# Kernel tuning notes

Hardware: AMD Instinct MI355X
Metric: run time of the kernel (lower is better)

Reference implementation:

```python
import jax, jax.numpy as jnp
import numpy as np

N, E, D, L, B = 50000, 800000, 128, 3, 256
BN_EPS = 1e-5


def _bn(h, g, b):
    # BatchNorm1d training-mode math over the node axis (biased variance)
    mu = jnp.mean(h, axis=0)
    var = jnp.mean(jnp.square(h - mu), axis=0)
    return (h - mu) * jax.lax.rsqrt(var + BN_EPS) * g + b


def setup_inputs() -> dict:
    key = jax.random.key(0)
    ks = jax.random.split(key, 6)
    scale = 1.0 / np.sqrt(D).astype(np.float32)
    return {
        "x": jax.random.normal(ks[0], (N, D), dtype=jnp.float32),
        "edge_index": jax.random.randint(ks[1], (2, E), 0, N, dtype=jnp.int32),
        "batch": jnp.sort(jax.random.randint(ks[2], (N,), 0, B, dtype=jnp.int32)),
        "W1": jax.random.normal(ks[3], (L, D, D), dtype=jnp.float32) * scale,
        "b1": jnp.zeros((L, D), jnp.float32),
        "g1": jnp.ones((L, D), jnp.float32),
        "be1": jnp.zeros((L, D), jnp.float32),
        "W2": jax.random.normal(ks[4], (L, D, D), dtype=jnp.float32) * scale,
        "b2": jnp.zeros((L, D), jnp.float32),
        "g2": jnp.ones((L, D), jnp.float32),
        "be2": jnp.zeros((L, D), jnp.float32),
    }


def reference(x, edge_index, batch, W1, b1, g1, be1, W2, b2, g2, be2):
    src, dst = edge_index[0], edge_index[1]
    h = x
    for i in range(L):
        # GINConv (eps=0): h' = nn((1+eps)*h + sum_{j in N(i)} h_j)
        agg = jax.ops.segment_sum(h[src], dst, num_segments=N)  # [N, D]
        h = h + agg
        # nn_layer: Linear -> BN -> ReLU -> Linear
        h = jax.nn.relu(_bn(h @ W1[i] + b1[i], g1[i], be1[i])) @ W2[i] + b2[i]
        # outer BatchNorm + ReLU (dropout is identity in eval)
        h = jax.nn.relu(_bn(h, g2[i], be2[i]))
    # global_add_pool over graphs
    return jax.ops.segment_sum(h, batch, num_segments=B)  # [B, D]
```

## Files before the change

kernel.cpp:

```cpp
#include <hip/hip_runtime.h>

constexpr int kN = 50000;
constexpr int kE = 800000;
constexpr int kD = 128;
constexpr int kB = 256;
constexpr int kL = 3;
constexpr float kEps = 1e-5f;

constexpr int kShift = 7;
constexpr int kNBuk = (kN + 127) >> 7;
constexpr int kEPB = 8192;
constexpr int kNBinBlk = (kE + kEPB - 1) / kEPB;

constexpr int kScanN = kN + 1;
constexpr int kScanGrid = (kScanN + 1023) / 1024;

constexpr int kPxc = kN * kD / 8;
constexpr int kPhist = kPxc + kE;
constexpr int kPbnd = kPhist + kN + 1;
constexpr int kPw1 = kPbnd + kL * kD * kD;
constexpr int kPw2 = kPw1 + kL * kD * kD;

typedef __attribute__((ext_vector_type(8))) short short8;
typedef __attribute__((ext_vector_type(4))) float f32x4;

__device__ __forceinline__ float4 bnrelu4(float4 v, float4 sc, float4 sh) {
  float4 r;
  r.x = fmaxf(fmaf(v.x, sc.x, sh.x), 0.f);
  r.y = fmaxf(fmaf(v.y, sc.y, sh.y), 0.f);
  r.z = fmaxf(fmaf(v.z, sc.z, sh.z), 0.f);
  r.w = fmaxf(fmaf(v.w, sc.w, sh.w), 0.f);
  return r;
}

__device__ __forceinline__ void acc4(float4& a, const float4& v) {
  a.x += v.x; a.y += v.y; a.z += v.z; a.w += v.w;
}
__device__ __forceinline__ void accsq4(float4& a, const float4& v) {
  a.x = fmaf(v.x, v.x, a.x); a.y = fmaf(v.y, v.y, a.y);
  a.z = fmaf(v.z, v.z, a.z); a.w = fmaf(v.w, v.w, a.w);
}

__device__ __forceinline__ unsigned int f2bf(float x) {
  unsigned int u = __float_as_uint(x);
  u = u + 0x7FFFu + ((u >> 16) & 1u);
  return u >> 16;
}
__device__ __forceinline__ float bf2f(unsigned int lo16) {
  return __uint_as_float(lo16 << 16);
}

__device__ __forceinline__ void bnmake(float su, float sq, float ga, float be,
                                       float& sc, float& sh) {
  float mu = su * (1.f / kN);
  float var = fmaf(-mu, mu, sq * (1.f / kN));
  float s = ga * rsqrtf(var + kEps);
  sc = s;
  sh = fmaf(-mu, s, be);
}

__global__ void k_prep(const float* __restrict__ x, const int* __restrict__ ei,
                       const int* __restrict__ bat, const float* __restrict__ W1,
                       const float* __restrict__ W2,
                       unsigned short* __restrict__ x16, int* __restrict__ rowptr,
                       int* __restrict__ gstart, unsigned short* __restrict__ Wf1,
                       unsigned short* __restrict__ Wf2) {
  int idx = blockIdx.x * 256 + threadIdx.x;
  if (idx < kPxc) {
    const float* ap = x + (size_t)idx * 8;
    float4 v0 = *reinterpret_cast<const float4*>(ap);
    float4 v1 = *reinterpret_cast<const float4*>(ap + 4);
    short8 u;
    u[0] = (short)f2bf(v0.x); u[1] = (short)f2bf(v0.y);
    u[2] = (short)f2bf(v0.z); u[3] = (short)f2bf(v0.w);
    u[4] = (short)f2bf(v1.x); u[5] = (short)f2bf(v1.y);
    u[6] = (short)f2bf(v1.z); u[7] = (short)f2bf(v1.w);
    *reinterpret_cast<short8*>(x16 + (size_t)idx * 8) = u;
  } else if (idx < kPhist) {
    int e = idx - kPxc;
    atomicAdd(&rowptr[1 + ei[kE + e]], 1);
  } else if (idx < kPbnd) {
    int n = idx - kPhist;
    int b = (n < kN) ? bat[n] : kB;
    int bp = (n > 0) ? bat[n - 1] : -1;
    for (int g = bp + 1; g <= b; ++g) gstart[g] = n;
  } else if (idx < kPw2) {
    const float* W = (idx < kPw1) ? W1 : W2;
    unsigned short* Wf = (idx < kPw1) ? Wf1 : Wf2;
    int id2 = idx - ((idx < kPw1) ? kPbnd : kPw1);
    int m = id2 & (kD * kD - 1);
    int w = id2 >> 14;
    int k = m >> 7, col = m & 127;
    int kb = k >> 5, cb = col >> 4;
    int lane = (col & 15) + 16 * ((k & 31) >> 3);
    int j = k & 7;
    Wf[(size_t)w * kD * kD + ((size_t)(kb * 8 + cb) * 64 + lane) * 8 + j] =
        (unsigned short)f2bf(W[id2]);
  }
}

__global__ __launch_bounds__(256) void k_scanA(int* __restrict__ data,
                                               int* __restrict__ partial) {
  __shared__ int wsum[4];
  const int tid = threadIdx.x;
  const int lane = tid & 63, wid = tid >> 6;
  const int base = blockIdx.x * 1024 + tid * 4;
  int4 v = make_int4(0, 0, 0, 0);
  if (base + 3 < kScanN) {
    v = *reinterpret_cast<const int4*>(data + base);
  } else if (base < kScanN) {
    v.x = data[base];
    if (base + 1 < kScanN) v.y = data[base + 1];
    if (base + 2 < kScanN) v.z = data[base + 2];
  }
  int s = v.x + v.y + v.z + v.w;
  int inc = s;
#pragma unroll
  for (int off = 1; off < 64; off <<= 1) {
    int t = __shfl_up(inc, off);
    if (lane >= off) inc += t;
  }
  if (lane == 63) wsum[wid] = inc;
  __syncthreads();
  int wpre = 0, total = 0;
#pragma unroll
  for (int k = 0; k < 4; ++k) {
    int t = wsum[k];
    if (k < wid) wpre += t;
    total += t;
  }
  if (tid == 0) partial[blockIdx.x] = total;
  int excl = wpre + inc - s;
  v.x += excl;
  v.y += v.x;
  v.z += v.y;
  v.w += v.z;
  if (base + 3 < kScanN) {
    *reinterpret_cast<int4*>(data + base) = v;
  } else if (base < kScanN) {
    data[base] = v.x;
    if (base + 1 < kScanN) data[base + 1] = v.y;
    if (base + 2 < kScanN) data[base + 2] = v.z;
  }
}

__global__ __launch_bounds__(256) void k_scanC(int* __restrict__ data,
                                               const int* __restrict__ partial,
                                               int* __restrict__ bcur) {
  const int b = blockIdx.x;
  const int tid = threadIdx.x;
  const int lane = tid & 63;
  int p = (lane < b) ? partial[lane] : 0;
#pragma unroll
  for (int off = 32; off; off >>= 1) p += __shfl_down(p, off);
  const int off0 = __shfl(p, 0);
  const int base = b * 1024 + tid * 4;
  if (base + 3 < kScanN) {
    int4 v = *reinterpret_cast<int4*>(data + base);
    v.x += off0; v.y += off0; v.z += off0; v.w += off0;
    *reinterpret_cast<int4*>(data + base) = v;
    if ((tid & 31) == 0) {
      int bk = b * 8 + (tid >> 5);
      if (bk < kNBuk) bcur[bk] = v.x;
    }
  } else if (base < kScanN) {
    for (int j = 0; j < 4 && base + j < kScanN; ++j) data[base + j] += off0;
  }
}

__global__ __launch_bounds__(256) void k_binpairs(
    const int* __restrict__ ei, int* __restrict__ bcur,
    unsigned int* __restrict__ pairs) {
  __shared__ int cnt[kNBuk];
  __shared__ int base[kNBuk];
  const int tid = threadIdx.x;
  const int e0 = blockIdx.x * kEPB;
  for (int t = tid; t < kNBuk; t += 256) cnt[t] = 0;
  __syncthreads();
  unsigned int dr[32];
#pragma unroll
  for (int i = 0; i < 32; ++i) {
    int e = e0 + i * 256 + tid;
    unsigned int v = 0xFFFFFFFFu;
    if (e < kE) {
      int d = ei[kE + e];
      int r = atomicAdd(&cnt[d >> kShift], 1);
      v = ((unsigned int)d << 16) | (unsigned int)r;
    }
    dr[i] = v;
  }
  __syncthreads();
  for (int t = tid; t < kNBuk; t += 256) {
    int c = cnt[t];
    base[t] = (c > 0) ? atomicAdd(&bcur[t], c) : 0;
  }
  __syncthreads();
#pragma unroll
  for (int i = 0; i < 32; ++i) {
    unsigned int v = dr[i];
    if (v == 0xFFFFFFFFu) continue;
    int e = e0 + i * 256 + tid;
    unsigned int s = (unsigned int)ei[e];
    int b = (int)(v >> 16) >> kShift;
    int pos = base[b] + (int)(v & 0xFFFFu);
    pairs[pos] = (v & 0xFFFF0000u) | s;
  }
}

__global__ __launch_bounds__(256) void k_csrfill(
    const unsigned int* __restrict__ pairs, const int* __restrict__ rowptr,
    int* __restrict__ srcs) {
  __shared__ int cur[128];
  const int b = blockIdx.x;
  const int tid = threadIdx.x;
  const int n0 = b << kShift;
  if (tid < 128) {
    int n = n0 + tid;
    cur[tid] = (n < kN) ? rowptr[n] : 0;
  }
  __syncthreads();
  const int pbeg = rowptr[n0];
  const int pend = rowptr[min(n0 + 128, kN)];
  for (int p = pbeg + tid; p < pend; p += 256) {
    unsigned int u = pairs[p];
    int local = (int)(u >> 16) - n0;
    int pos = atomicAdd(&cur[local], 1);
    srcs[pos] = (int)(u & 0xFFFFu);
  }
}

template <bool BN>
__global__ __launch_bounds__(256) void k_gather(
    const unsigned int* __restrict__ h16, const int* __restrict__ rowptr,
    const int* __restrict__ srcs, const float* __restrict__ stats,
    const float* __restrict__ gam, const float* __restrict__ bet,
    unsigned int* __restrict__ agg16) {
  const int node = blockIdx.x * 4 + (threadIdx.x >> 6);
  const int lane = threadIdx.x & 63;
  float scx, scy, shx, shy;
  if (BN) {
    int c = lane * 2;
    bnmake(stats[c], stats[kD + c], gam[c], bet[c], scx, shx);
    bnmake(stats[c + 1], stats[kD + c + 1], gam[c + 1], bet[c + 1], scy, shy);
  }
  unsigned int u = h16[(size_t)node * 64 + lane];
  float ax = bf2f(u & 0xFFFFu), ay = __uint_as_float(u & 0xFFFF0000u);
  if (BN) {
    ax = fmaxf(fmaf(ax, scx, shx), 0.f);
    ay = fmaxf(fmaf(ay, scy, shy), 0.f);
  }
  const int beg = __builtin_amdgcn_readfirstlane(rowptr[node]);
  const int end = __builtin_amdgcn_readfirstlane(rowptr[node + 1]);
  int j = beg;
  for (; j + 4 <= end; j += 4) {
    int s0 = srcs[j + 0];
    int s1 = srcs[j + 1];
    int s2 = srcs[j + 2];
    int s3 = srcs[j + 3];
    unsigned int v0 = h16[(size_t)s0 * 64 + lane];
    unsigned int v1 = h16[(size_t)s1 * 64 + lane];
    unsigned int v2 = h16[(size_t)s2 * 64 + lane];
    unsigned int v3 = h16[(size_t)s3 * 64 + lane];
    float x0 = bf2f(v0 & 0xFFFFu), y0 = __uint_as_float(v0 & 0xFFFF0000u);
    float x1 = bf2f(v1 & 0xFFFFu), y1 = __uint_as_float(v1 & 0xFFFF0000u);
    float x2 = bf2f(v2 & 0xFFFFu), y2 = __uint_as_float(v2 & 0xFFFF0000u);
    float x3 = bf2f(v3 & 0xFFFFu), y3 = __uint_as_float(v3 & 0xFFFF0000u);
    if (BN) {
      x0 = fmaxf(fmaf(x0, scx, shx), 0.f); y0 = fmaxf(fmaf(y0, scy, shy), 0.f);
      x1 = fmaxf(fmaf(x1, scx, shx), 0.f); y1 = fmaxf(fmaf(y1, scy, shy), 0.f);
      x2 = fmaxf(fmaf(x2, scx, shx), 0.f); y2 = fmaxf(fmaf(y2, scy, shy), 0.f);
      x3 = fmaxf(fmaf(x3, scx, shx), 0.f); y3 = fmaxf(fmaf(y3, scy, shy), 0.f);
    }
    ax += (x0 + x1) + (x2 + x3);
    ay += (y0 + y1) + (y2 + y3);
  }
  for (; j < end; ++j) {
    int s = srcs[j];
    unsigned int v = h16[(size_t)s * 64 + lane];
    float vx = bf2f(v & 0xFFFFu), vy = __uint_as_float(v & 0xFFFF0000u);
    if (BN) {
      vx = fmaxf(fmaf(vx, scx, shx), 0.f);
      vy = fmaxf(fmaf(vy, scy, shy), 0.f);
    }
    ax += vx;
    ay += vy;
  }
  agg16[(size_t)node * 64 + lane] = f2bf(ax) | (f2bf(ay) << 16);
}

__global__ __launch_bounds__(256) void k_gemm(
    const unsigned short* __restrict__ A16, const unsigned short* __restrict__ Wf,
    const float* __restrict__ bias, const float* __restrict__ statsA,
    const float* __restrict__ gamA, const float* __restrict__ betA,
    unsigned short* __restrict__ Y16,
    float* __restrict__ s_sum, float* __restrict__ s_ss) {
  union SMem {
    unsigned short af[32 * 64 * 8];
    float epi[64 * 132];
  };
  __shared__ SMem sm;

  const int tid = threadIdx.x;
  const int w = tid >> 6;
  const int lane = tid & 63;
  const int row0 = blockIdx.x * 128;

  short8 bfr[4][2];
#pragma unroll
  for (int kb = 0; kb < 4; ++kb)
#pragma unroll
    for (int c = 0; c < 2; ++c)
      bfr[kb][c] = *reinterpret_cast<const short8*>(
          Wf + ((size_t)(kb * 8 + (2 * w + c)) * 64 + lane) * 8);

  {
    const int rlow = tid >> 4;
    const int k0 = (tid & 15) * 8;
    const int kb = k0 >> 5;
    const int lif = rlow + 16 * ((k0 & 31) >> 3);
    float4 sc0, sc1, sh0, sh1;
    if (statsA != nullptr) {
      float4 su0 = *reinterpret_cast<const float4*>(statsA + k0);
      float4 su1 = *reinterpret_cast<const float4*>(statsA + k0 + 4);
      float4 sq0 = *reinterpret_cast<const float4*>(statsA + kD + k0);
      float4 sq1 = *reinterpret_cast<const float4*>(statsA + kD + k0 + 4);
      float4 ga0 = *reinterpret_cast<const float4*>(gamA + k0);
      float4 ga1 = *reinterpret_cast<const float4*>(gamA + k0 + 4);
      float4 be0 = *reinterpret_cast<const float4*>(betA + k0);
      float4 be1 = *reinterpret_cast<const float4*>(betA + k0 + 4);
      bnmake(su0.x, sq0.x, ga0.x, be0.x, sc0.x, sh0.x);
      bnmake(su0.y, sq0.y, ga0.y, be0.y, sc0.y, sh0.y);
      bnmake(su0.z, sq0.z, ga0.z, be0.z, sc0.z, sh0.z);
      bnmake(su0.w, sq0.w, ga0.w, be0.w, sc0.w, sh0.w);
      bnmake(su1.x, sq1.x, ga1.x, be1.x, sc1.x, sh1.x);
      bnmake(su1.y, sq1.y, ga1.y, be1.y, sc1.y, sh1.y);
      bnmake(su1.z, sq1.z, ga1.z, be1.z, sc1.z, sh1.z);
      bnmake(su1.w, sq1.w, ga1.w, be1.w, sc1.w, sh1.w);
    }
#pragma unroll
    for (int i = 0; i < 8; ++i) {
      int grow = row0 + rlow + 16 * i;
      short8 u = (short8)0;
      if (grow < kN) {
        u = *reinterpret_cast<const short8*>(A16 + (size_t)grow * kD + k0);
        if (statsA != nullptr) {
          float4 v0, v1;
          v0.x = bf2f((unsigned short)u[0]); v0.y = bf2f((unsigned short)u[1]);
          v0.z = bf2f((unsigned short)u[2]); v0.w = bf2f((unsigned short)u[3]);
          v1.x = bf2f((unsigned short)u[4]); v1.y = bf2f((unsigned short)u[5]);
          v1.z = bf2f((unsigned short)u[6]); v1.w = bf2f((unsigned short)u[7]);
          v0 = bnrelu4(v0, sc0, sh0);
          v1 = bnrelu4(v1, sc1, sh1);
          u[0] = (short)f2bf(v0.x); u[1] = (short)f2bf(v0.y);
          u[2] = (short)f2bf(v0.z); u[3] = (short)f2bf(v0.w);
          u[4] = (short)f2bf(v1.x); u[5] = (short)f2bf(v1.y);
          u[6] = (short)f2bf(v1.z); u[7] = (short)f2bf(v1.w);
        }
      }
      int frag = i * 4 + kb;
      *reinterpret_cast<short8*>(&sm.af[((size_t)frag * 64 + lif) * 8]) = u;
    }
  }
  __syncthreads();

  f32x4 acc[8][2];
#pragma unroll
  for (int rb = 0; rb < 8; ++rb) {
    acc[rb][0] = (f32x4){0.f, 0.f, 0.f, 0.f};
    acc[rb][1] = (f32x4){0.f, 0.f, 0.f, 0.f};
  }
#pragma unroll
  for (int kb = 0; kb < 4; ++kb) {
    short8 afr[8];
#pragma unroll
    for (int rb = 0; rb < 8; ++rb)
      afr[rb] = *reinterpret_cast<const short8*>(
          &sm.af[((size_t)(rb * 4 + kb) * 64 + lane) * 8]);
#pragma unroll
    for (int rb = 0; rb < 8; ++rb) {
      acc[rb][0] = __builtin_amdgcn_mfma_f32_16x16x32_bf16(afr[rb], bfr[kb][0],
                                                           acc[rb][0], 0, 0, 0);
      acc[rb][1] = __builtin_amdgcn_mfma_f32_16x16x32_bf16(afr[rb], bfr[kb][1],
                                                           acc[rb][1], 0, 0, 0);
    }
  }

  const int col4 = tid & 31;
  const int rowg = tid >> 5;
  float4 b4 = reinterpret_cast<const float4*>(bias)[col4];
  float4 ss = make_float4(0.f, 0.f, 0.f, 0.f);
  float4 qq = make_float4(0.f, 0.f, 0.f, 0.f);

#pragma unroll
  for (int p = 0; p < 2; ++p) {
    __syncthreads();
#pragma unroll
    for (int rb4 = 0; rb4 < 4; ++rb4) {
      int rb = p * 4 + rb4;
#pragma unroll
      for (int c = 0; c < 2; ++c) {
#pragma unroll
        for (int j = 0; j < 4; ++j) {
          sm.epi[(size_t)(rb4 * 16 + (lane >> 4) * 4 + j) * 132 +
                 w * 32 + c * 16 + (lane & 15)] = acc[rb][c][j];
        }
      }
    }
    __syncthreads();
#pragma unroll
    for (int i = 0; i < 8; ++i) {
      int lrow = rowg * 8 + i;
      int grow = row0 + p * 64 + lrow;
      float4 v = *reinterpret_cast<float4*>(&sm.epi[(size_t)lrow * 132 + col4 * 4]);
      acc4(v, b4);
      if (grow < kN) {
        uint2 pk;
        pk.x = f2bf(v.x) | (f2bf(v.y) << 16);
        pk.y = f2bf(v.z) | (f2bf(v.w) << 16);
        *reinterpret_cast<uint2*>(Y16 + (size_t)grow * kD + col4 * 4) = pk;
        acc4(ss, v);
        accsq4(qq, v);
      }
    }
  }

  __syncthreads();
  *reinterpret_cast<float4*>(&sm.epi[(size_t)rowg * 128 + col4 * 4]) = ss;
  *reinterpret_cast<float4*>(&sm.epi[1024 + (size_t)rowg * 128 + col4 * 4]) = qq;
  __syncthreads();
  if (tid < kD) {
    float s = 0.f;
#pragma unroll
    for (int j = 0; j < 8; ++j) s += sm.epi[j * 128 + tid];
    atomicAdd(&s_sum[tid], s);
  } else {
    int c = tid - kD;
    float s = 0.f;
#pragma unroll
    for (int j = 0; j < 8; ++j) s += sm.epi[1024 + j * 128 + c];
    atomicAdd(&s_ss[c], s);
  }
}

__global__ __launch_bounds__(256) void k_pool(
    const unsigned short* __restrict__ h16, const int* __restrict__ gstart,
    const float* __restrict__ stats, const float* __restrict__ gam,
    const float* __restrict__ bet, float* __restrict__ out) {
  const int g = blockIdx.x;
  const int q = threadIdx.x & 31;
  const int r = threadIdx.x >> 5;
  const int s = gstart[g], e = gstart[g + 1];
  float4 sc, sh;
  {
    int c = q * 4;
    bnmake(stats[c + 0], stats[kD + c + 0], gam[c + 0], bet[c + 0], sc.x, sh.x);
    bnmake(stats[c + 1], stats[kD + c + 1], gam[c + 1], bet[c + 1], sc.y, sh.y);
    bnmake(stats[c + 2], stats[kD + c + 2], gam[c + 2], bet[c + 2], sc.z, sh.z);
    bnmake(stats[c + 3], stats[kD + c + 3], gam[c + 3], bet[c + 3], sc.w, sh.w);
  }
  float4 acc = make_float4(0.f, 0.f, 0.f, 0.f);
  for (int n = s + r; n < e; n += 8) {
    uint2 u = *reinterpret_cast<const uint2*>(h16 + (size_t)n * kD + q * 4);
    float4 v;
    v.x = bf2f(u.x & 0xFFFFu);
    v.y = __uint_as_float(u.x & 0xFFFF0000u);
    v.z = bf2f(u.y & 0xFFFFu);
    v.w = __uint_as_float(u.y & 0xFFFF0000u);
    acc4(acc, bnrelu4(v, sc, sh));
  }
  __shared__ float4 red[8][32];
  red[r][q] = acc;
  __syncthreads();
  if (r == 0) {
    float4 t = acc;
#pragma unroll
    for (int j = 1; j < 8; ++j) acc4(t, red[j][q]);
    reinterpret_cast<float4*>(out)[(size_t)g * 32 + q] = t;
  }
}

extern "C" void kernel_launch(void* const* d_in, const int* in_sizes, int n_in,
                              void* d_out, int out_size, void* d_ws, size_t ws_size,
                              hipStream_t stream) {
  const float* x   = (const float*)d_in[0];
  const int*   ei  = (const int*)d_in[1];
  const int*   bat = (const int*)d_in[2];
  const float* W1  = (const float*)d_in[3];
  const float* b1  = (const float*)d_in[4];
  const float* g1  = (const float*)d_in[5];
  const float* be1 = (const float*)d_in[6];
  const float* W2  = (const float*)d_in[7];
  const float* b2  = (const float*)d_in[8];
  const float* g2  = (const float*)d_in[9];
  const float* be2 = (const float*)d_in[10];
  float* out = (float*)d_out;

  char* p = (char*)d_ws;
  float* wsf = (float*)p;                       p += 16384;
  unsigned short* x16 = (unsigned short*)p;     p += (size_t)kN * kD * 2;
  unsigned short* bufA = (unsigned short*)p;    p += (size_t)kN * kD * 2;
  unsigned short* bufB = (unsigned short*)p;    p += (size_t)kN * kD * 2;
  unsigned short* Wf1 = (unsigned short*)p;     p += (size_t)kL * kD * kD * 2;
  unsigned short* Wf2 = (unsigned short*)p;     p += (size_t)kL * kD * kD * 2;
  int* rowptr = (int*)p;                        p += (kN + 2) * 4;
  int* bcur = (int*)p;                          p += (kNBuk + 1) * 4;
  int* partial = (int*)p;                       p += 64 * 4;
  int* gstart = (int*)p;                        p += (kB + 2) * 4;
  unsigned int* pairs = (unsigned int*)p;       p += (size_t)kE * 4;
  int* srcs = (int*)p;                          p += (size_t)kE * 4;

  (void)hipMemsetAsync(wsf, 0, 6 * 512 * sizeof(float), stream);
  (void)hipMemsetAsync(rowptr, 0, (kN + 1) * sizeof(int), stream);

  k_prep<<<(kPw2 + 255) / 256, 256, 0, stream>>>(x, ei, bat, W1, W2, x16, rowptr,
                                                 gstart, Wf1, Wf2);
  k_scanA<<<kScanGrid, 256, 0, stream>>>(rowptr, partial);
  k_scanC<<<kScanGrid, 256, 0, stream>>>(rowptr, partial, bcur);
  k_binpairs<<<kNBinBlk, 256, 0, stream>>>(ei, bcur, pairs);
  k_csrfill<<<kNBuk, 256, 0, stream>>>(pairs, rowptr, srcs);

  const unsigned short* curH = x16;
  const float* curStats = nullptr;
  const float* curGam = nullptr;
  const float* curBet = nullptr;
  const int ngemm = (kN + 127) / 128;

  unsigned short* aggBuf = bufA;
  unsigned short* yBuf = bufB;

  for (int l = 0; l < kL; ++l) {
    if (curStats == nullptr)
      k_gather<false><<<kN / 4, 256, 0, stream>>>(
          (const unsigned int*)curH, rowptr, srcs, nullptr, nullptr, nullptr,
          (unsigned int*)aggBuf);
    else
      k_gather<true><<<kN / 4, 256, 0, stream>>>(
          (const unsigned int*)curH, rowptr, srcs, curStats, curGam, curBet,
          (unsigned int*)aggBuf);

    float* st1 = wsf + (size_t)(l * 2 + 0) * 512;
    k_gemm<<<ngemm, 256, 0, stream>>>(aggBuf, Wf1 + (size_t)l * kD * kD,
                                      b1 + l * kD, nullptr, nullptr, nullptr,
                                      yBuf, st1, st1 + kD);

    float* st2 = wsf + (size_t)(l * 2 + 1) * 512;
    k_gemm<<<ngemm, 256, 0, stream>>>(yBuf, Wf2 + (size_t)l * kD * kD,
                                      b2 + l * kD, st1, g1 + l * kD, be1 + l * kD,
                                      aggBuf, st2, st2 + kD);

    curH = aggBuf;
    curStats = st2;
    curGam = g2 + l * kD;
    curBet = be2 + l * kD;
    unsigned short* tmp = aggBuf;
    aggBuf = yBuf;
    yBuf = tmp;
  }

  k_pool<<<kB, 256, 0, stream>>>(curH, gstart, curStats, curGam, curBet, out);
}
```

Measured before the change: 321.8 us.

## Build CSR via bucket histogram and per-bucket local scan instead of global node histogram

Replaces the per-edge global atomic histogram over all nodes and the two-pass global scan with a shared-memory bucket histogram (128 nodes per bucket), a single-block scan over buckets, and per-node counting plus a local scan inside csrfill that writes rowptr. This removes 800K global atomics, one memset of rowptr, and one kernel launch. It adds a second read of the pairs array in csrfill and blocks in k_prep that rescan edges.

```diff
diff --git a/kernel.cpp b/kernel.cpp
--- a/kernel.cpp
+++ b/kernel.cpp
@@ -12,14 +12,11 @@
 constexpr int kEPB = 8192;
 constexpr int kNBinBlk = (kE + kEPB - 1) / kEPB;
 
-constexpr int kScanN = kN + 1;
-constexpr int kScanGrid = (kScanN + 1023) / 1024;
-
 constexpr int kPxc = kN * kD / 8;
-constexpr int kPhist = kPxc + kE;
-constexpr int kPbnd = kPhist + kN + 1;
+constexpr int kPbnd = kPxc + kN + 1;
 constexpr int kPw1 = kPbnd + kL * kD * kD;
 constexpr int kPw2 = kPw1 + kL * kD * kD;
+constexpr int kPrepThreadBlks = (kPw2 + 255) / 256;
 
 typedef __attribute__((ext_vector_type(8))) short short8;
 typedef __attribute__((ext_vector_type(4))) float f32x4;
@@ -59,13 +56,31 @@
   sh = fmaf(-mu, s, be);
 }
 
-__global__ void k_prep(const float* __restrict__ x, const int* __restrict__ ei,
-                       const int* __restrict__ bat, const float* __restrict__ W1,
-                       const float* __restrict__ W2,
-                       unsigned short* __restrict__ x16, int* __restrict__ rowptr,
-                       int* __restrict__ gstart, unsigned short* __restrict__ Wf1,
-                       unsigned short* __restrict__ Wf2) {
-  int idx = blockIdx.x * 256 + threadIdx.x;
+__global__ __launch_bounds__(256) void k_prep(
+    const float* __restrict__ x, const int* __restrict__ ei,
+    const int* __restrict__ bat, const float* __restrict__ W1,
+    const float* __restrict__ W2, unsigned short* __restrict__ x16,
+    int* __restrict__ bhist, int* __restrict__ gstart,
+    unsigned short* __restrict__ Wf1, unsigned short* __restrict__ Wf2) {
+  __shared__ int cnt[kNBuk];
+  if (blockIdx.x < (unsigned)kNBinBlk) {
+    const int tid = threadIdx.x;
+    const int e0 = blockIdx.x * kEPB;
+    for (int t = tid; t < kNBuk; t += 256) cnt[t] = 0;
+    __syncthreads();
+#pragma unroll
+    for (int i = 0; i < 32; ++i) {
+      int e = e0 + i * 256 + tid;
+      if (e < kE) atomicAdd(&cnt[ei[kE + e] >> kShift], 1);
+    }
+    __syncthreads();
+    for (int t = tid; t < kNBuk; t += 256) {
+      int c = cnt[t];
+      if (c) atomicAdd(&bhist[t], c);
+    }
+    return;
+  }
+  int idx = (blockIdx.x - kNBinBlk) * 256 + threadIdx.x;
   if (idx < kPxc) {
     const float* ap = x + (size_t)idx * 8;
     float4 v0 = *reinterpret_cast<const float4*>(ap);
@@ -76,11 +91,8 @@
     u[4] = (short)f2bf(v1.x); u[5] = (short)f2bf(v1.y);
     u[6] = (short)f2bf(v1.z); u[7] = (short)f2bf(v1.w);
     *reinterpret_cast<short8*>(x16 + (size_t)idx * 8) = u;
-  } else if (idx < kPhist) {
-    int e = idx - kPxc;
-    atomicAdd(&rowptr[1 + ei[kE + e]], 1);
   } else if (idx < kPbnd) {
-    int n = idx - kPhist;
+    int n = idx - kPxc;
     int b = (n < kN) ? bat[n] : kB;
     int bp = (n > 0) ? bat[n - 1] : -1;
     for (int g = bp + 1; g <= b; ++g) gstart[g] = n;
@@ -99,22 +111,14 @@
   }
 }
 
-__global__ __launch_bounds__(256) void k_scanA(int* __restrict__ data,
-                                               int* __restrict__ partial) {
-  __shared__ int wsum[4];
+__global__ __launch_bounds__(512) void k_scanB(const int* __restrict__ bhist,
+                                               int* __restrict__ bstart,
+                                               int* __restrict__ bcur) {
+  __shared__ int wsum[8];
   const int tid = threadIdx.x;
   const int lane = tid & 63, wid = tid >> 6;
-  const int base = blockIdx.x * 1024 + tid * 4;
-  int4 v = make_int4(0, 0, 0, 0);
-  if (base + 3 < kScanN) {
-    v = *reinterpret_cast<const int4*>(data + base);
-  } else if (base < kScanN) {
-    v.x = data[base];
-    if (base + 1 < kScanN) v.y = data[base + 1];
-    if (base + 2 < kScanN) v.z = data[base + 2];
-  }
-  int s = v.x + v.y + v.z + v.w;
-  int inc = s;
+  int v = (tid < kNBuk) ? bhist[tid] : 0;
+  int inc = v;
 #pragma unroll
   for (int off = 1; off < 64; off <<= 1) {
     int t = __shfl_up(inc, off);
@@ -122,49 +126,16 @@
   }
   if (lane == 63) wsum[wid] = inc;
   __syncthreads();
-  int wpre = 0, total = 0;
-#pragma unroll
-  for (int k = 0; k < 4; ++k) {
+  int wpre = 0;
+#pragma unroll
+  for (int k = 0; k < 8; ++k) {
     int t = wsum[k];
     if (k < wid) wpre += t;
-    total += t;
-  }
-  if (tid == 0) partial[blockIdx.x] = total;
-  int excl = wpre + inc - s;
-  v.x += excl;
-  v.y += v.x;
-  v.z += v.y;
-  v.w += v.z;
-  if (base + 3 < kScanN) {
-    *reinterpret_cast<int4*>(data + base) = v;
-  } else if (base < kScanN) {
-    data[base] = v.x;
-    if (base + 1 < kScanN) data[base + 1] = v.y;
-    if (base + 2 < kScanN) data[base + 2] = v.z;
-  }
-}
-
-__global__ __launch_bounds__(256) void k_scanC(int* __restrict__ data,
-                                               const int* __restrict__ partial,
-                                               int* __restrict__ bcur) {
-  const int b = blockIdx.x;
-  const int tid = threadIdx.x;
-  const int lane = tid & 63;
-  int p = (lane < b) ? partial[lane] : 0;
-#pragma unroll
-  for (int off = 32; off; off >>= 1) p += __shfl_down(p, off);
-  const int off0 = __shfl(p, 0);
-  const int base = b * 1024 + tid * 4;
-  if (base + 3 < kScanN) {
-    int4 v = *reinterpret_cast<int4*>(data + base);
-    v.x += off0; v.y += off0; v.z += off0; v.w += off0;
-    *reinterpret_cast<int4*>(data + base) = v;
-    if ((tid & 31) == 0) {
-      int bk = b * 8 + (tid >> 5);
-      if (bk < kNBuk) bcur[bk] = v.x;
-    }
-  } else if (base < kScanN) {
-    for (int j = 0; j < 4 && base + j < kScanN; ++j) data[base + j] += off0;
+  }
+  int excl = wpre + inc - v;
+  if (tid <= kNBuk) {
+    bstart[tid] = excl;
+    if (tid < kNBuk) bcur[tid] = excl;
   }
 }
 
@@ -208,20 +179,41 @@
 }
 
 __global__ __launch_bounds__(256) void k_csrfill(
-    const unsigned int* __restrict__ pairs, const int* __restrict__ rowptr,
-    int* __restrict__ srcs) {
+    const unsigned int* __restrict__ pairs, const int* __restrict__ bstart,
+    int* __restrict__ rowptr, int* __restrict__ srcs) {
+  __shared__ int cnt[128];
   __shared__ int cur[128];
+  __shared__ int w0tot;
   const int b = blockIdx.x;
   const int tid = threadIdx.x;
   const int n0 = b << kShift;
+  const int pb = bstart[b];
+  const int pe = bstart[b + 1];
+  if (tid < 128) cnt[tid] = 0;
+  __syncthreads();
+  for (int p = pb + tid; p < pe; p += 256)
+    atomicAdd(&cnt[(int)(pairs[p] >> 16) - n0], 1);
+  __syncthreads();
+  int v = 0, inc = 0;
   if (tid < 128) {
+    v = cnt[tid];
+    inc = v;
+#pragma unroll
+    for (int off = 1; off < 64; off <<= 1) {
+      int t = __shfl_up(inc, off);
+      if ((tid & 63) >= off) inc += t;
+    }
+    if (tid == 63) w0tot = inc;
+  }
+  __syncthreads();
+  if (tid < 128) {
+    int excl = inc - v + ((tid >= 64) ? w0tot : 0);
     int n = n0 + tid;
-    cur[tid] = (n < kN) ? rowptr[n] : 0;
-  }
-  __syncthreads();
-  const int pbeg = rowptr[n0];
-  const int pend = rowptr[min(n0 + 128, kN)];
-  for (int p = pbeg + tid; p < pend; p += 256) {
+    if (n <= kN) rowptr[n] = pb + excl;
+    cur[tid] = pb + excl;
+  }
+  __syncthreads();
+  for (int p = pb + tid; p < pe; p += 256) {
     unsigned int u = pairs[p];
     int local = (int)(u >> 16) - n0;
     int pos = atomicAdd(&cur[local], 1);
@@ -503,21 +495,21 @@
   unsigned short* Wf1 = (unsigned short*)p;     p += (size_t)kL * kD * kD * 2;
   unsigned short* Wf2 = (unsigned short*)p;     p += (size_t)kL * kD * kD * 2;
   int* rowptr = (int*)p;                        p += (kN + 2) * 4;
+  int* bhist = (int*)p;                         p += (kNBuk + 1) * 4;
+  int* bstart = (int*)p;                        p += (kNBuk + 1) * 4;
   int* bcur = (int*)p;                          p += (kNBuk + 1) * 4;
-  int* partial = (int*)p;                       p += 64 * 4;
   int* gstart = (int*)p;                        p += (kB + 2) * 4;
   unsigned int* pairs = (unsigned int*)p;       p += (size_t)kE * 4;
   int* srcs = (int*)p;                          p += (size_t)kE * 4;
 
   (void)hipMemsetAsync(wsf, 0, 6 * 512 * sizeof(float), stream);
-  (void)hipMemsetAsync(rowptr, 0, (kN + 1) * sizeof(int), stream);
-
-  k_prep<<<(kPw2 + 255) / 256, 256, 0, stream>>>(x, ei, bat, W1, W2, x16, rowptr,
-                                                 gstart, Wf1, Wf2);
-  k_scanA<<<kScanGrid, 256, 0, stream>>>(rowptr, partial);
-  k_scanC<<<kScanGrid, 256, 0, stream>>>(rowptr, partial, bcur);
+  (void)hipMemsetAsync(bhist, 0, kNBuk * sizeof(int), stream);
+
+  k_prep<<<kNBinBlk + kPrepThreadBlks, 256, 0, stream>>>(x, ei, bat, W1, W2, x16,
+                                                         bhist, gstart, Wf1, Wf2);
+  k_scanB<<<1, 512, 0, stream>>>(bhist, bstart, bcur);
   k_binpairs<<<kNBinBlk, 256, 0, stream>>>(ei, bcur, pairs);
-  k_csrfill<<<kNBuk, 256, 0, stream>>>(pairs, rowptr, srcs);
+  k_csrfill<<<kNBuk, 256, 0, stream>>>(pairs, bstart, rowptr, srcs);
 
   const unsigned short* curH = x16;
   const float* curStats = nullptr;
```

Measured after the change: 293.6 us. 8.8% less time.
